# Performance work log

Hardware: AMD Instinct MI355X
Metric: run time of the kernel (lower is better)

## Reference

```python
import jax, jax.numpy as jnp
import numpy as np

C = 512
CI = C // 4  # inter_channels
EPS = 1e-5


def _conv1x1(x, w, b):
    # x: [B,C,H,W], w: [O,C], b: [O] -> [B,O,H,W]
    return jnp.einsum('bchw,oc->bohw', x, w) + b[None, :, None, None]


def _maxpool2(t):
    # 2x2 max pool, stride 2 (NCHW)
    b, c, h, w = t.shape
    return t.reshape(b, c, h // 2, 2, w // 2, 2).max(axis=(3, 5))


def setup_inputs() -> dict:
    key = jax.random.key(0)
    ks = jax.random.split(key, 9)
    B, H, W = 8, 64, 64
    s_in = 1.0 / np.sqrt(C)
    s_ci = 1.0 / np.sqrt(CI)
    return {
        'x': jax.random.normal(ks[0], (B, C, H, W), jnp.float32),
        'g_w': jax.random.normal(ks[1], (CI, C), jnp.float32) * s_in,
        'g_b': jnp.zeros((CI,), jnp.float32),
        'phi_w': jax.random.normal(ks[2], (CI, C), jnp.float32) * s_in,
        'phi_b': jnp.zeros((CI,), jnp.float32),
        'theta_w': jax.random.normal(ks[3], (CI, C), jnp.float32) * s_in,
        'theta_b': jnp.zeros((CI,), jnp.float32),
        'W_w': jax.random.normal(ks[4], (C, CI), jnp.float32) * s_ci,
        'W_b': jnp.zeros((C,), jnp.float32),
        'ln_gamma': jax.random.normal(ks[5], (C,), jnp.float32) * 0.02 + 1.0,
        'ln_beta': jnp.zeros((C,), jnp.float32),
    }


def reference(x, g_w, g_b, phi_w, phi_b, theta_w, theta_b, W_w, W_b, ln_gamma, ln_beta):
    B, Cc, H, Wd = x.shape
    N = H * Wd
    # projections; g and phi are maxpool-downsampled (N/4 key/value positions)
    g_x = _maxpool2(_conv1x1(x, g_w, g_b)).reshape(B, CI, N // 4)          # [B,Ci,M]
    phi_x = _maxpool2(_conv1x1(x, phi_w, phi_b)).reshape(B, CI, N // 4)    # [B,Ci,M]
    theta_x = _conv1x1(x, theta_w, theta_b).reshape(B, CI, N)              # [B,Ci,N]
    # attention: QK^T -> softmax -> V
    f = jnp.einsum('bcn,bcm->bnm', theta_x, phi_x)                          # [B,N,M]
    attn = jax.nn.softmax(f, axis=-1)
    y = jnp.einsum('bnm,bcm->bcn', attn, g_x).reshape(B, CI, H, Wd)         # [B,Ci,H,W]
    # output projection + channels-first LayerNorm + residual
    W_y = _conv1x1(y, W_w, W_b)                                             # [B,C,H,W]
    mu = W_y.mean(axis=1, keepdims=True)
    var = W_y.var(axis=1, keepdims=True)
    W_y = (W_y - mu) * jax.lax.rsqrt(var + EPS)
    W_y = W_y * ln_gamma[None, :, None, None] + ln_beta[None, :, None, None]
    return W_y + x
```

## Files before the change

### kernel.cpp

```cpp
#include <hip/hip_runtime.h>
#include <math.h>

constexpr int Cc  = 512;
constexpr int CIc = 128;
constexpr int Bc  = 8;
constexpr int Nc  = 4096;
constexpr int Mc  = 1024;

typedef __bf16 bf16x8 __attribute__((ext_vector_type(8)));
typedef float  f32x4  __attribute__((ext_vector_type(4)));

__device__ __forceinline__ unsigned short f2bf(float f) {
  unsigned u = __float_as_uint(f);
  u += 0x7fffu + ((u >> 16) & 1u);
  return (unsigned short)(u >> 16);
}
__device__ __forceinline__ float bf2f(unsigned short h) {
  return __uint_as_float((unsigned)h << 16);
}
__device__ __forceinline__ unsigned pack2bf(float lo, float hi) {
  return (unsigned)f2bf(lo) | ((unsigned)f2bf(hi) << 16);
}

__device__ __forceinline__ void gload16(const void* g, void* lds) {
  __builtin_amdgcn_global_load_lds(
      (const __attribute__((address_space(1))) unsigned int*)g,
      (__attribute__((address_space(3))) unsigned int*)lds, 16, 0, 0);
}

__global__ __launch_bounds__(256) void k_prep(
    const float* __restrict__ gw, const float* __restrict__ pw,
    const float* __restrict__ tw, const float* __restrict__ Ww,
    const float* __restrict__ gb, const float* __restrict__ pb,
    const float* __restrict__ tb,
    unsigned short* __restrict__ wcat, unsigned short* __restrict__ wwb,
    float* __restrict__ bcat) {
  int i = blockIdx.x * 256 + threadIdx.x;
  if (i < 49152) {
    int c = i >> 7, q = i & 127;
    const float* src = (c < 128) ? tw + (size_t)c * 512
                     : (c < 256) ? pw + (size_t)(c - 128) * 512
                                 : gw + (size_t)(c - 256) * 512;
    float4 v = *(const float4*)(src + q * 4);
    ushort4 o;
    o.x = f2bf(v.x); o.y = f2bf(v.y); o.z = f2bf(v.z); o.w = f2bf(v.w);
    *(ushort4*)(wcat + (size_t)c * 512 + q * 4) = o;
  } else if (i < 65536) {
    int i2 = i - 49152;
    int c = i2 >> 5, q = i2 & 31;
    float4 v = *(const float4*)(Ww + (size_t)c * 128 + q * 4);
    ushort4 o;
    o.x = f2bf(v.x); o.y = f2bf(v.y); o.z = f2bf(v.z); o.w = f2bf(v.w);
    *(ushort4*)(wwb + (size_t)c * 128 + q * 4) = o;
  } else if (i < 65920) {
    int j = i - 65536;
    bcat[j] = (j < 128) ? tb[j] : (j < 256) ? pb[j - 128] : gb[j - 256];
  }
}

__global__ __launch_bounds__(512) void k_conv_all(
    const float* __restrict__ x, const unsigned short* __restrict__ wcat,
    const float* __restrict__ bcat,
    unsigned short* __restrict__ theta_t, unsigned short* __restrict__ pf,
    unsigned short* __restrict__ gf) {
  __shared__ __align__(16) char smem[98304];
  const int b = blockIdx.y, n0 = blockIdx.x * 128;
  const int t = threadIdx.x;
  const int w = t >> 6, l = t & 63, lr = l & 15, lg = l >> 4;

  const char* wsrc = (const char*)wcat;
  int woff[6];
#pragma unroll
  for (int i = 0; i < 6; ++i) {
    int r = (w * 6 + i) * 8 + (l >> 3);
    woff[i] = r * 1024 + (((l & 7) * 16) ^ ((r & 7) << 4));
  }

  const float* xb = x + (size_t)b * Cc * Nc + n0 + w * 16 + lr;

  float xraw[16];
#define LOADX(k0_)                                                        \
  {                                                                       \
    _Pragma("unroll")                                                     \
    for (int ks = 0; ks < 2; ++ks)                                        \
      _Pragma("unroll")                                                   \
      for (int j = 0; j < 8; ++j)                                         \
        xraw[ks * 8 + j] = xb[(size_t)((k0_) + ks * 32 + lg * 8 + j) * Nc]; \
  }
#define STAGEW(buf_, k0_)                                                 \
  {                                                                       \
    char* dst_ = smem + (buf_) * 49152;                                   \
    _Pragma("unroll")                                                     \
    for (int i = 0; i < 6; ++i)                                           \
      gload16(wsrc + (size_t)(k0_) * 2 + woff[i], dst_ + (w * 6 + i) * 1024); \
  }

  f32x4 acc[24];
#pragma unroll
  for (int tc = 0; tc < 24; ++tc) acc[tc] = (f32x4){0.f, 0.f, 0.f, 0.f};

  LOADX(0);
  STAGEW(0, 0);
  asm volatile("s_waitcnt vmcnt(0)" ::: "memory");
  __builtin_amdgcn_s_barrier();

  for (int c = 0; c < 8; ++c) {
    const int cur = c & 1;
    bf16x8 af[2];
#pragma unroll
    for (int ks = 0; ks < 2; ++ks) {
      union { unsigned u[4]; bf16x8 v; } ab;
#pragma unroll
      for (int q = 0; q < 4; ++q)
        ab.u[q] = pack2bf(xraw[ks * 8 + 2 * q], xraw[ks * 8 + 2 * q + 1]);
      af[ks] = ab.v;
    }
    if (c < 7) {
      LOADX((c + 1) * 64);
      STAGEW(cur ^ 1, (c + 1) * 64);
    }
    const char* Wb = smem + cur * 49152;
    __builtin_amdgcn_s_setprio(1);
#pragma unroll
    for (int ks = 0; ks < 2; ++ks)
#pragma unroll
      for (int tc = 0; tc < 24; ++tc) {
        int r = tc * 16 + lr;
        bf16x8 bfr = *(const bf16x8*)(
            Wb + r * 128 + ((lg * 16 + ks * 64) ^ ((lr & 7) << 4)));
        acc[tc] = __builtin_amdgcn_mfma_f32_16x16x32_bf16(af[ks], bfr, acc[tc], 0, 0, 0);
      }
    __builtin_amdgcn_s_setprio(0);
    asm volatile("s_waitcnt vmcnt(0)" ::: "memory");
    __builtin_amdgcn_s_barrier();
  }
#undef LOADX
#undef STAGEW

  unsigned short* Ys = (unsigned short*)smem;
#pragma unroll
  for (int h = 0; h < 2; ++h) {
    __syncthreads();
    if ((w >> 2) == h) {
      int rw = (w & 3) * 16;
#pragma unroll
      for (int tc = 0; tc < 24; ++tc) {
        float bv = bcat[tc * 16 + lr];
#pragma unroll
        for (int reg = 0; reg < 4; ++reg)
          Ys[(rw + lg * 4 + reg) * 408 + tc * 16 + lr] = f2bf(acc[tc][reg] + bv);
      }
    }
    __syncthreads();
#pragma unroll
    for (int buf = 0; buf < 3; ++buf) {
      unsigned short* dst = (buf == 0) ? theta_t : (buf == 1) ? pf : gf;
#pragma unroll
      for (int it = 0; it < 2; ++it) {
        int idx = it * 512 + t;
        int n = idx >> 4, j = idx & 15;
        bf16x8 v = *(const bf16x8*)(Ys + n * 408 + buf * 128 + j * 8);
        *(bf16x8*)(dst + (((size_t)(b * Nc + n0 + h * 64 + n)) << 7) + j * 8) = v;
      }
    }
  }
}

__global__ __launch_bounds__(256) void k_pool(
    const unsigned short* __restrict__ pf, const unsigned short* __restrict__ gf,
    unsigned short* __restrict__ phi_t, unsigned short* __restrict__ gbuf) {
  __shared__ unsigned short T[128 * 33];
  const int h2 = blockIdx.x, b = blockIdx.y;
  const int t = threadIdx.x;
  const int ml = t >> 3, j0 = t & 7;
  const size_t base = ((size_t)(b * Nc + h2 * 128 + 2 * ml)) << 7;
#pragma unroll
  for (int half = 0; half < 2; ++half) {
    const int j = j0 + half * 8;
    {
      bf16x8 a = *(const bf16x8*)(pf + base + j * 8);
      bf16x8 c = *(const bf16x8*)(pf + base + 128 + j * 8);
      bf16x8 d = *(const bf16x8*)(pf + base + 64 * 128 + j * 8);
      bf16x8 e = *(const bf16x8*)(pf + base + 65 * 128 + j * 8);
      const unsigned short *pa = (const unsigned short*)&a, *pc = (const unsigned short*)&c,
                           *pd = (const unsigned short*)&d, *pe = (const unsigned short*)&e;
      unsigned short o[8];
#pragma unroll
      for (int q = 0; q < 8; ++q) {
        float m0 = fmaxf(fmaxf(bf2f(pa[q]), bf2f(pc[q])), fmaxf(bf2f(pd[q]), bf2f(pe[q])));
        o[q] = f2bf(m0);
      }
      ushort4 o0, o1;
      o0.x = o[0]; o0.y = o[1]; o0.z = o[2]; o0.w = o[3];
      o1.x = o[4]; o1.y = o[5]; o1.z = o[6]; o1.w = o[7];
      unsigned short* dp = phi_t + (((size_t)(b * Mc + h2 * 32 + ml)) << 7) + j * 8;
      *(ushort4*)dp = o0;
      *(ushort4*)(dp + 4) = o1;
    }
    {
      bf16x8 a = *(const bf16x8*)(gf + base + j * 8);
      bf16x8 c = *(const bf16x8*)(gf + base + 128 + j * 8);
      bf16x8 d = *(const bf16x8*)(gf + base + 64 * 128 + j * 8);
      bf16x8 e = *(const bf16x8*)(gf + base + 65 * 128 + j * 8);
      const unsigned short *pa = (const unsigned short*)&a, *pc = (const unsigned short*)&c,
                           *pd = (const unsigned short*)&d, *pe = (const unsigned short*)&e;
#pragma unroll
      for (int q = 0; q < 8; ++q) {
        float m0 = fmaxf(fmaxf(bf2f(pa[q]), bf2f(pc[q])), fmaxf(bf2f(pd[q]), bf2f(pe[q])));
        T[(j * 8 + q) * 33 + ml] = f2bf(m0);
      }
    }
  }
  __syncthreads();
  {
    int ci = t >> 1, half = t & 1;
    unsigned short tmp[16];
#pragma unroll
    for (int q = 0; q < 16; ++q) tmp[q] = T[ci * 33 + half * 16 + q];
    unsigned short* dst = gbuf + ((size_t)(b * CIc + ci)) * Mc + h2 * 32 + half * 16;
    *(ushort4*)(dst + 0)  = *(ushort4*)(tmp + 0);
    *(ushort4*)(dst + 4)  = *(ushort4*)(tmp + 4);
    *(ushort4*)(dst + 8)  = *(ushort4*)(tmp + 8);
    *(ushort4*)(dst + 12) = *(ushort4*)(tmp + 12);
  }
}

__global__ __launch_bounds__(256) void k_attn_mfma(
    const unsigned short* __restrict__ theta_t,
    const unsigned short* __restrict__ phi_t,
    const unsigned short* __restrict__ gv,
    unsigned short* __restrict__ y_t) {
  __shared__ __align__(16) char Kb[2][16384];
  __shared__ __align__(16) char Vb[2][16384];
  __shared__ __align__(16) unsigned short Ps[4][16][72];
  const int b = blockIdx.y, n0 = blockIdx.x * 64;
  const int tid = threadIdx.x;
  const int w = tid >> 6, l = tid & 63;
  const int lr = l & 15, lg = l >> 4;

  const int krow_l = l >> 4, kchunk = (l & 15) * 16;
  const int vrow_l = l >> 3, vchunk = (l & 7) * 16;
  int koff[4], voff[4];
#pragma unroll
  for (int i = 0; i < 4; ++i) {
    int kr = w * 16 + i * 4 + krow_l;
    koff[i] = kr * 256 + (kchunk ^ ((kr & 7) << 4));
    int vr = w * 32 + i * 8 + vrow_l;
    voff[i] = vr * 2048 + (vchunk ^ ((vr & 7) << 4));
  }
  const char* kbase = (const char*)(phi_t + (((size_t)(b * Mc)) << 7));
  const char* vbase = (const char*)(gv + (((size_t)b) << 17));

  auto stage = [&](int buf, int t) {
#pragma unroll
    for (int i = 0; i < 4; ++i)
      gload16(kbase + t * 16384 + koff[i], &Kb[buf][(w * 4 + i) * 1024]);
#pragma unroll
    for (int i = 0; i < 4; ++i)
      gload16(vbase + t * 128 + voff[i], &Vb[buf][(w * 4 + i) * 1024]);
  };

  bf16x8 qf[4];
  {
    const unsigned short* qp =
        theta_t + (((size_t)(b * Nc + n0 + w * 16 + lr)) << 7);
#pragma unroll
    for (int kk = 0; kk < 4; ++kk)
      qf[kk] = *(const bf16x8*)(qp + kk * 32 + lg * 8);
  }
  f32x4 of[8];
#pragma unroll
  for (int ct = 0; ct < 8; ++ct) of[ct] = (f32x4){0.f, 0.f, 0.f, 0.f};
  float run_m[4], run_l[4];
#pragma unroll
  for (int r = 0; r < 4; ++r) { run_m[r] = -1e30f; run_l[r] = 0.f; }

  stage(0, 0);
  asm volatile("s_waitcnt vmcnt(0)" ::: "memory");
  __builtin_amdgcn_s_barrier();

  for (int t = 0; t < Mc / 64; ++t) {
    const int cur = t & 1;
    if (t + 1 < Mc / 64) stage(cur ^ 1, t + 1);
    const char* Ks = Kb[cur];
    const char* Vs = Vb[cur];
    f32x4 sm[4];
    __builtin_amdgcn_s_setprio(1);
#pragma unroll
    for (int mt = 0; mt < 4; ++mt) {
      f32x4 s = (f32x4){0.f, 0.f, 0.f, 0.f};
#pragma unroll
      for (int kk = 0; kk < 4; ++kk) {
        bf16x8 kf = *(const bf16x8*)(
            Ks + (mt * 16 + lr) * 256 + ((kk * 64 + lg * 16) ^ ((lr & 7) << 4)));
        s = __builtin_amdgcn_mfma_f32_16x16x32_bf16(qf[kk], kf, s, 0, 0, 0);
      }
      sm[mt] = s;
    }
    __builtin_amdgcn_s_setprio(0);
#pragma unroll
    for (int reg = 0; reg < 4; ++reg) {
      float mx = fmaxf(fmaxf(sm[0][reg], sm[1][reg]), fmaxf(sm[2][reg], sm[3][reg]));
      mx = fmaxf(mx, __shfl_xor(mx, 1));
      mx = fmaxf(mx, __shfl_xor(mx, 2));
      mx = fmaxf(mx, __shfl_xor(mx, 4));
      mx = fmaxf(mx, __shfl_xor(mx, 8));
      float nm = fmaxf(run_m[reg], mx);
      float sc = __expf(run_m[reg] - nm);
      run_m[reg] = nm;
      float rs = 0.f;
#pragma unroll
      for (int mt = 0; mt < 4; ++mt) {
        float p = __expf(sm[mt][reg] - nm);
        Ps[w][lg * 4 + reg][mt * 16 + lr] = f2bf(p);
        rs += p;
      }
      rs += __shfl_xor(rs, 1);
      rs += __shfl_xor(rs, 2);
      rs += __shfl_xor(rs, 4);
      rs += __shfl_xor(rs, 8);
      run_l[reg] = run_l[reg] * sc + rs;
#pragma unroll
      for (int ct = 0; ct < 8; ++ct) of[ct][reg] *= sc;
    }
    bf16x8 pa0 = *(const bf16x8*)(&Ps[w][lr][lg * 8]);
    bf16x8 pa1 = *(const bf16x8*)(&Ps[w][lr][32 + lg * 8]);
    __builtin_amdgcn_s_setprio(1);
#pragma unroll
    for (int ct = 0; ct < 8; ++ct) {
      bf16x8 vf0 = *(const bf16x8*)(
          Vs + (ct * 16 + lr) * 128 + ((lg * 16) ^ ((lr & 7) << 4)));
      of[ct] = __builtin_amdgcn_mfma_f32_16x16x32_bf16(pa0, vf0, of[ct], 0, 0, 0);
      bf16x8 vf1 = *(const bf16x8*)(
          Vs + (ct * 16 + lr) * 128 + ((64 + lg * 16) ^ ((lr & 7) << 4)));
      of[ct] = __builtin_amdgcn_mfma_f32_16x16x32_bf16(pa1, vf1, of[ct], 0, 0, 0);
    }
    __builtin_amdgcn_s_setprio(0);
    asm volatile("s_waitcnt vmcnt(0)" ::: "memory");
    __builtin_amdgcn_s_barrier();
  }
  float invl[4];
#pragma unroll
  for (int reg = 0; reg < 4; ++reg) invl[reg] = 1.f / run_l[reg];
  unsigned short* Ys = (unsigned short*)Kb;
#pragma unroll
  for (int ct = 0; ct < 8; ++ct)
#pragma unroll
    for (int reg = 0; reg < 4; ++reg)
      Ys[(w * 16 + lg * 4 + reg) * 128 + ct * 16 + lr] =
          f2bf(of[ct][reg] * invl[reg]);
  __syncthreads();
#pragma unroll
  for (int it = 0; it < 4; ++it) {
    int i = it * 256 + tid;
    int r = i >> 4, cl = i & 15;
    *(bf16x8*)(y_t + (((size_t)(b * Nc + n0 + r)) << 7) + cl * 8) =
        *(const bf16x8*)(Ys + r * 128 + cl * 8);
  }
}

__global__ __launch_bounds__(256) void k_wconv_mfma(
    const unsigned short* __restrict__ y_t, const unsigned short* __restrict__ wwb,
    const float* __restrict__ wbias, const float* __restrict__ gamma,
    const float* __restrict__ beta, const float* __restrict__ x,
    float* __restrict__ out) {
  __shared__ __align__(16) char smem[36864];
  unsigned short* WTs = (unsigned short*)smem;
  float* Ys = (float*)smem;
  const int b = blockIdx.y, n0 = blockIdx.x * 64;
  const int t = threadIdx.x;
  const int w = t >> 6, l = t & 63, lr = l & 15, lg = l >> 4;

  bf16x8 qf[4];
  {
    const unsigned short* qp = y_t + (((size_t)(b * Nc + n0 + w * 16 + lr)) << 7);
#pragma unroll
    for (int kk = 0; kk < 4; ++kk)
      qf[kk] = *(const bf16x8*)(qp + kk * 32 + lg * 8);
  }
  f32x4 acc[32];
#pragma unroll
  for (int i = 0; i < 32; ++i) acc[i] = (f32x4){0.f, 0.f, 0.f, 0.f};

#pragma unroll
  for (int cc = 0; cc < 4; ++cc) {
    __syncthreads();
#pragma unroll
    for (int it = 0; it < 8; ++it) {
      int i = it * 256 + t;
      int r = i >> 4, j = i & 15;
      bf16x8 v = *(const bf16x8*)(wwb + (((size_t)(cc * 128 + r)) << 7) + j * 8);
      *(bf16x8*)((char*)WTs + r * 256 + ((j * 16) ^ ((r & 7) << 4))) = v;
    }
    __syncthreads();
#pragma unroll
    for (int tc = 0; tc < 8; ++tc) {
      f32x4 a = acc[cc * 8 + tc];
      int r = tc * 16 + lr;
#pragma unroll
      for (int kk = 0; kk < 4; ++kk) {
        bf16x8 kf = *(const bf16x8*)(
            (char*)WTs + r * 256 + ((kk * 64 + lg * 16) ^ ((lr & 7) << 4)));
        a = __builtin_amdgcn_mfma_f32_16x16x32_bf16(qf[kk], kf, a, 0, 0, 0);
      }
      acc[cc * 8 + tc] = a;
    }
  }
  float s[4] = {0.f, 0.f, 0.f, 0.f}, q[4] = {0.f, 0.f, 0.f, 0.f};
#pragma unroll
  for (int cc = 0; cc < 4; ++cc)
#pragma unroll
    for (int tc = 0; tc < 8; ++tc) {
      float wb = wbias[cc * 128 + tc * 16 + lr];
      f32x4 a = acc[cc * 8 + tc];
#pragma unroll
      for (int reg = 0; reg < 4; ++reg) {
        a[reg] += wb;
        s[reg] += a[reg];
        q[reg] += a[reg] * a[reg];
      }
      acc[cc * 8 + tc] = a;
    }
  float mu[4], rs[4];
#pragma unroll
  for (int reg = 0; reg < 4; ++reg) {
    float sv = s[reg], qv = q[reg];
    sv += __shfl_xor(sv, 1); qv += __shfl_xor(qv, 1);
    sv += __shfl_xor(sv, 2); qv += __shfl_xor(qv, 2);
    sv += __shfl_xor(sv, 4); qv += __shfl_xor(qv, 4);
    sv += __shfl_xor(sv, 8); qv += __shfl_xor(qv, 8);
    mu[reg] = sv * (1.f / 512.f);
    float var = qv * (1.f / 512.f) - mu[reg] * mu[reg];
    rs[reg] = rsqrtf(var + 1e-5f);
  }
#pragma unroll
  for (int cc = 0; cc < 4; ++cc) {
    __syncthreads();
#pragma unroll
    for (int tc = 0; tc < 8; ++tc) {
      int c = cc * 128 + tc * 16 + lr;
      float ga = gamma[c], be = beta[c];
#pragma unroll
      for (int reg = 0; reg < 4; ++reg)
        Ys[(tc * 16 + lr) * 72 + w * 16 + lg * 4 + reg] =
            (acc[cc * 8 + tc][reg] - mu[reg]) * rs[reg] * ga + be;
    }
    __syncthreads();
#pragma unroll
    for (int it = 0; it < 8; ++it) {
      int idx = it * 256 + t;
      int r = idx >> 4, j = idx & 15;
      float4 v = *(const float4*)&Ys[r * 72 + j * 4];
      size_t gaddr = ((size_t)b * Cc + cc * 128 + r) * Nc + n0 + j * 4;
      float4 xv = *(const float4*)&x[gaddr];
      float4 o;
      o.x = v.x + xv.x; o.y = v.y + xv.y; o.z = v.z + xv.z; o.w = v.w + xv.w;
      *(float4*)&out[gaddr] = o;
    }
  }
}

extern "C" void kernel_launch(void* const* d_in, const int* in_sizes, int n_in,
                              void* d_out, int out_size, void* d_ws, size_t ws_size,
                              hipStream_t stream) {
  const float* x       = (const float*)d_in[0];
  const float* g_w     = (const float*)d_in[1];
  const float* g_b     = (const float*)d_in[2];
  const float* phi_w   = (const float*)d_in[3];
  const float* phi_b   = (const float*)d_in[4];
  const float* theta_w = (const float*)d_in[5];
  const float* theta_b = (const float*)d_in[6];
  const float* W_w     = (const float*)d_in[7];
  const float* W_b     = (const float*)d_in[8];
  const float* ln_g    = (const float*)d_in[9];
  const float* ln_b    = (const float*)d_in[10];
  float* out = (float*)d_out;

  unsigned short* theta_t = (unsigned short*)d_ws;
  unsigned short* pf      = theta_t + (size_t)Bc * Nc * CIc;
  unsigned short* gf      = pf + (size_t)Bc * Nc * CIc;
  unsigned short* y_t     = gf + (size_t)Bc * Nc * CIc;
  unsigned short* phi_t   = y_t + (size_t)Bc * Nc * CIc;
  unsigned short* gbuf    = phi_t + (size_t)Bc * Mc * CIc;
  unsigned short* wcat    = gbuf + (size_t)Bc * Mc * CIc;
  unsigned short* wwb     = wcat + (size_t)384 * 512;
  float*          bcat    = (float*)(wwb + (size_t)512 * 128);

  k_prep<<<dim3(258), dim3(256), 0, stream>>>(
      g_w, phi_w, theta_w, W_w, g_b, phi_b, theta_b, wcat, wwb, bcat);
  k_conv_all<<<dim3(Nc / 128, Bc), dim3(512), 0, stream>>>(
      x, wcat, bcat, theta_t, pf, gf);
  k_pool<<<dim3(32, Bc), dim3(256), 0, stream>>>(pf, gf, phi_t, gbuf);
  k_attn_mfma<<<dim3(Nc / 64, Bc), dim3(256), 0, stream>>>(
      theta_t, phi_t, gbuf, y_t);
  k_wconv_mfma<<<dim3(Nc / 64, Bc), dim3(256), 0, stream>>>(
      y_t, wwb, W_b, ln_g, ln_b, x, out);
}
```

Measured before the change: 119.3 us.

## Fuse maxpool into projection conv and use lazy softmax rescaling in attention

The 2x2 max-pool of the phi and g projections now happens inside k_conv_all, working from shared memory, so the separate k_pool kernel and the full-resolution pf/gf intermediates in global memory go away. This removes one launch and a large write-then-read round trip through HBM. The attention kernel now rescales the running max, sum and output accumulators only when some row's block max exceeds the running max by more than 8. It also packs P to bf16 with v_cvt_pk_bf16_f32, cutting per-tile exp and scaling work in exchange for a looser but still safe bound on exponent growth.

New measurement: 112.6 us. 1.06x faster.

```diff
diff --git a/kernel.cpp b/kernel.cpp
--- a/kernel.cpp
+++ b/kernel.cpp
@@ -61,10 +61,10 @@
 __global__ __launch_bounds__(512) void k_conv_all(
     const float* __restrict__ x, const unsigned short* __restrict__ wcat,
     const float* __restrict__ bcat,
-    unsigned short* __restrict__ theta_t, unsigned short* __restrict__ pf,
-    unsigned short* __restrict__ gf) {
+    unsigned short* __restrict__ theta_t, unsigned short* __restrict__ phi_t,
+    unsigned short* __restrict__ gbuf) {
   __shared__ __align__(16) char smem[98304];
-  const int b = blockIdx.y, n0 = blockIdx.x * 128;
+  const int b = blockIdx.y, h2 = blockIdx.x, n0 = h2 * 128;
   const int t = threadIdx.x;
   const int w = t >> 6, l = t & 63, lr = l & 15, lg = l >> 4;
 
@@ -137,91 +137,82 @@
 #undef LOADX
 #undef STAGEW
 
-  unsigned short* Ys = (unsigned short*)smem;
-#pragma unroll
-  for (int h = 0; h < 2; ++h) {
-    __syncthreads();
-    if ((w >> 2) == h) {
-      int rw = (w & 3) * 16;
-#pragma unroll
-      for (int tc = 0; tc < 24; ++tc) {
-        float bv = bcat[tc * 16 + lr];
-#pragma unroll
-        for (int reg = 0; reg < 4; ++reg)
-          Ys[(rw + lg * 4 + reg) * 408 + tc * 16 + lr] = f2bf(acc[tc][reg] + bv);
-      }
-    }
-    __syncthreads();
-#pragma unroll
-    for (int buf = 0; buf < 3; ++buf) {
-      unsigned short* dst = (buf == 0) ? theta_t : (buf == 1) ? pf : gf;
-#pragma unroll
-      for (int it = 0; it < 2; ++it) {
-        int idx = it * 512 + t;
-        int n = idx >> 4, j = idx & 15;
-        bf16x8 v = *(const bf16x8*)(Ys + n * 408 + buf * 128 + j * 8);
-        *(bf16x8*)(dst + (((size_t)(b * Nc + n0 + h * 64 + n)) << 7) + j * 8) = v;
-      }
-    }
-  }
-}
-
-__global__ __launch_bounds__(256) void k_pool(
-    const unsigned short* __restrict__ pf, const unsigned short* __restrict__ gf,
-    unsigned short* __restrict__ phi_t, unsigned short* __restrict__ gbuf) {
-  __shared__ unsigned short T[128 * 33];
-  const int h2 = blockIdx.x, b = blockIdx.y;
-  const int t = threadIdx.x;
-  const int ml = t >> 3, j0 = t & 7;
-  const size_t base = ((size_t)(b * Nc + h2 * 128 + 2 * ml)) << 7;
-#pragma unroll
-  for (int half = 0; half < 2; ++half) {
-    const int j = j0 + half * 8;
-    {
-      bf16x8 a = *(const bf16x8*)(pf + base + j * 8);
-      bf16x8 c = *(const bf16x8*)(pf + base + 128 + j * 8);
-      bf16x8 d = *(const bf16x8*)(pf + base + 64 * 128 + j * 8);
-      bf16x8 e = *(const bf16x8*)(pf + base + 65 * 128 + j * 8);
-      const unsigned short *pa = (const unsigned short*)&a, *pc = (const unsigned short*)&c,
-                           *pd = (const unsigned short*)&d, *pe = (const unsigned short*)&e;
-      unsigned short o[8];
-#pragma unroll
-      for (int q = 0; q < 8; ++q) {
-        float m0 = fmaxf(fmaxf(bf2f(pa[q]), bf2f(pc[q])), fmaxf(bf2f(pd[q]), bf2f(pe[q])));
-        o[q] = f2bf(m0);
-      }
-      ushort4 o0, o1;
-      o0.x = o[0]; o0.y = o[1]; o0.z = o[2]; o0.w = o[3];
-      o1.x = o[4]; o1.y = o[5]; o1.z = o[6]; o1.w = o[7];
-      unsigned short* dp = phi_t + (((size_t)(b * Mc + h2 * 32 + ml)) << 7) + j * 8;
-      *(ushort4*)dp = o0;
-      *(ushort4*)(dp + 4) = o1;
-    }
-    {
-      bf16x8 a = *(const bf16x8*)(gf + base + j * 8);
-      bf16x8 c = *(const bf16x8*)(gf + base + 128 + j * 8);
-      bf16x8 d = *(const bf16x8*)(gf + base + 64 * 128 + j * 8);
-      bf16x8 e = *(const bf16x8*)(gf + base + 65 * 128 + j * 8);
-      const unsigned short *pa = (const unsigned short*)&a, *pc = (const unsigned short*)&c,
-                           *pd = (const unsigned short*)&d, *pe = (const unsigned short*)&e;
-#pragma unroll
-      for (int q = 0; q < 8; ++q) {
-        float m0 = fmaxf(fmaxf(bf2f(pa[q]), bf2f(pc[q])), fmaxf(bf2f(pd[q]), bf2f(pe[q])));
-        T[(j * 8 + q) * 33 + ml] = f2bf(m0);
-      }
+  unsigned short* PG = (unsigned short*)smem;
+  unsigned short* Yt = (unsigned short*)(smem + 67584);
+  const int rbase = w * 16 + lg * 4;
+
+#pragma unroll
+  for (int tc = 8; tc < 24; ++tc) {
+    float bv = bcat[tc * 16 + lr];
+#pragma unroll
+    for (int reg = 0; reg < 4; ++reg)
+      PG[(rbase + reg) * 264 + tc * 16 + lr - 128] = f2bf(acc[tc][reg] + bv);
+  }
+  if (w < 4) {
+#pragma unroll
+    for (int tc = 0; tc < 8; ++tc) {
+      float bv = bcat[tc * 16 + lr];
+#pragma unroll
+      for (int reg = 0; reg < 4; ++reg)
+        Yt[(rbase + reg) * 136 + tc * 16 + lr] = f2bf(acc[tc][reg] + bv);
     }
   }
   __syncthreads();
+#pragma unroll
+  for (int it = 0; it < 2; ++it) {
+    int idx = it * 512 + t, n = idx >> 4, j = idx & 15;
+    *(bf16x8*)(theta_t + (((size_t)(b * Nc + n0 + n)) << 7) + j * 8) =
+        *(const bf16x8*)(Yt + n * 136 + j * 8);
+  }
   {
-    int ci = t >> 1, half = t & 1;
-    unsigned short tmp[16];
-#pragma unroll
-    for (int q = 0; q < 16; ++q) tmp[q] = T[ci * 33 + half * 16 + q];
-    unsigned short* dst = gbuf + ((size_t)(b * CIc + ci)) * Mc + h2 * 32 + half * 16;
-    *(ushort4*)(dst + 0)  = *(ushort4*)(tmp + 0);
-    *(ushort4*)(dst + 4)  = *(ushort4*)(tmp + 4);
-    *(ushort4*)(dst + 8)  = *(ushort4*)(tmp + 8);
-    *(ushort4*)(dst + 12) = *(ushort4*)(tmp + 12);
+    int mloc = t >> 4, j = t & 15;
+    const unsigned short* r0 = &PG[(2 * mloc) * 264 + j * 8];
+    const unsigned short* r1 = &PG[(2 * mloc + 1) * 264 + j * 8];
+    const unsigned short* r2 = &PG[(64 + 2 * mloc) * 264 + j * 8];
+    const unsigned short* r3 = &PG[(65 + 2 * mloc) * 264 + j * 8];
+    unsigned short o[8];
+#pragma unroll
+    for (int q = 0; q < 8; ++q)
+      o[q] = f2bf(fmaxf(fmaxf(bf2f(r0[q]), bf2f(r1[q])),
+                        fmaxf(bf2f(r2[q]), bf2f(r3[q]))));
+    unsigned short* dp = phi_t + (((size_t)(b * Mc + h2 * 32 + mloc)) << 7) + j * 8;
+    *(ushort4*)dp = *(ushort4*)o;
+    *(ushort4*)(dp + 4) = *(ushort4*)(o + 4);
+  }
+  {
+    int ci = t >> 2, mq = t & 3;
+    unsigned short tmp[8];
+#pragma unroll
+    for (int q = 0; q < 8; ++q) {
+      int w2 = mq * 8 + q;
+      float m0 = fmaxf(
+          fmaxf(bf2f(PG[(2 * w2) * 264 + 128 + ci]),
+                bf2f(PG[(2 * w2 + 1) * 264 + 128 + ci])),
+          fmaxf(bf2f(PG[(64 + 2 * w2) * 264 + 128 + ci]),
+                bf2f(PG[(65 + 2 * w2) * 264 + 128 + ci])));
+      tmp[q] = f2bf(m0);
+    }
+    unsigned short* dst = gbuf + ((size_t)(b * CIc + ci)) * Mc + h2 * 32 + mq * 8;
+    *(ushort4*)(dst) = *(ushort4*)(tmp);
+    *(ushort4*)(dst + 4) = *(ushort4*)(tmp + 4);
+  }
+  __syncthreads();
+  if (w >= 4) {
+#pragma unroll
+    for (int tc = 0; tc < 8; ++tc) {
+      float bv = bcat[tc * 16 + lr];
+#pragma unroll
+      for (int reg = 0; reg < 4; ++reg)
+        Yt[((w - 4) * 16 + lg * 4 + reg) * 136 + tc * 16 + lr] =
+            f2bf(acc[tc][reg] + bv);
+    }
+  }
+  __syncthreads();
+#pragma unroll
+  for (int it = 0; it < 2; ++it) {
+    int idx = it * 512 + t, n = idx >> 4, j = idx & 15;
+    *(bf16x8*)(theta_t + (((size_t)(b * Nc + n0 + 64 + n)) << 7) + j * 8) =
+        *(const bf16x8*)(Yt + n * 136 + j * 8);
   }
 }
 
@@ -298,6 +289,7 @@
       sm[mt] = s;
     }
     __builtin_amdgcn_s_setprio(0);
+    float pmax[4];
 #pragma unroll
     for (int reg = 0; reg < 4; ++reg) {
       float mx = fmaxf(fmaxf(sm[0][reg], sm[1][reg]), fmaxf(sm[2][reg], sm[3][reg]));
@@ -305,23 +297,41 @@
       mx = fmaxf(mx, __shfl_xor(mx, 2));
       mx = fmaxf(mx, __shfl_xor(mx, 4));
       mx = fmaxf(mx, __shfl_xor(mx, 8));
-      float nm = fmaxf(run_m[reg], mx);
-      float sc = __expf(run_m[reg] - nm);
-      run_m[reg] = nm;
-      float rs = 0.f;
-#pragma unroll
-      for (int mt = 0; mt < 4; ++mt) {
-        float p = __expf(sm[mt][reg] - nm);
-        Ps[w][lg * 4 + reg][mt * 16 + lr] = f2bf(p);
-        rs += p;
+      pmax[reg] = mx;
+    }
+    bool need = (pmax[0] > run_m[0] + 8.f) | (pmax[1] > run_m[1] + 8.f) |
+                (pmax[2] > run_m[2] + 8.f) | (pmax[3] > run_m[3] + 8.f);
+    if (__any(need)) {
+#pragma unroll
+      for (int reg = 0; reg < 4; ++reg) {
+        float nm = fmaxf(run_m[reg], pmax[reg]);
+        float sc = __expf(run_m[reg] - nm);
+        run_m[reg] = nm;
+        run_l[reg] *= sc;
+#pragma unroll
+        for (int ct = 0; ct < 8; ++ct) of[ct][reg] *= sc;
       }
+    }
+#pragma unroll
+    for (int reg = 0; reg < 4; ++reg) {
+      float p0 = __expf(sm[0][reg] - run_m[reg]);
+      float p1 = __expf(sm[1][reg] - run_m[reg]);
+      float p2 = __expf(sm[2][reg] - run_m[reg]);
+      float p3 = __expf(sm[3][reg] - run_m[reg]);
+      unsigned pk01, pk23;
+      asm("v_cvt_pk_bf16_f32 %0, %1, %2" : "=v"(pk01) : "v"(p0), "v"(p1));
+      asm("v_cvt_pk_bf16_f32 %0, %1, %2" : "=v"(pk23) : "v"(p2), "v"(p3));
+      unsigned short* pr = &Ps[w][lg * 4 + reg][lr];
+      pr[0]  = (unsigned short)pk01;
+      pr[16] = (unsigned short)(pk01 >> 16);
+      pr[32] = (unsigned short)pk23;
+      pr[48] = (unsigned short)(pk23 >> 16);
+      float rs = (p0 + p1) + (p2 + p3);
       rs += __shfl_xor(rs, 1);
       rs += __shfl_xor(rs, 2);
       rs += __shfl_xor(rs, 4);
       rs += __shfl_xor(rs, 8);
-      run_l[reg] = run_l[reg] * sc + rs;
-#pragma unroll
-      for (int ct = 0; ct < 8; ++ct) of[ct][reg] *= sc;
+      run_l[reg] += rs;
     }
     bf16x8 pa0 = *(const bf16x8*)(&Ps[w][lr][lg * 8]);
     bf16x8 pa1 = *(const bf16x8*)(&Ps[w][lr][32 + lg * 8]);
@@ -477,9 +487,7 @@
   float* out = (float*)d_out;
 
   unsigned short* theta_t = (unsigned short*)d_ws;
-  unsigned short* pf      = theta_t + (size_t)Bc * Nc * CIc;
-  unsigned short* gf      = pf + (size_t)Bc * Nc * CIc;
-  unsigned short* y_t     = gf + (size_t)Bc * Nc * CIc;
+  unsigned short* y_t     = theta_t + (size_t)Bc * Nc * CIc;
   unsigned short* phi_t   = y_t + (size_t)Bc * Nc * CIc;
   unsigned short* gbuf    = phi_t + (size_t)Bc * Mc * CIc;
   unsigned short* wcat    = gbuf + (size_t)Bc * Mc * CIc;
@@ -489,8 +497,7 @@
   k_prep<<<dim3(258), dim3(256), 0, stream>>>(
       g_w, phi_w, theta_w, W_w, g_b, phi_b, theta_b, wcat, wwb, bcat);
   k_conv_all<<<dim3(Nc / 128, Bc), dim3(512), 0, stream>>>(
-      x, wcat, bcat, theta_t, pf, gf);
-  k_pool<<<dim3(32, Bc), dim3(256), 0, stream>>>(pf, gf, phi_t, gbuf);
+      x, wcat, bcat, theta_t, phi_t, gbuf);
   k_attn_mfma<<<dim3(Nc / 64, Bc), dim3(256), 0, stream>>>(
       theta_t, phi_t, gbuf, y_t);
   k_wconv_mfma<<<dim3(Nc / 64, Bc), dim3(256), 0, stream>>>(
```
